# Kernel optimization log

Measured on AMD Instinct MI355X. Metric: run time of the kernel, lower is better.

Reference implementation:

```python
import jax, jax.numpy as jnp
import numpy as np

NUM_ITEMS = 50000
NUM_USERS = 16384   # static number of user segments (total_user universe)
H0 = 512            # encoder_hidden_size[0]
LAT = 256           # bottleneck (encoder_hidden_size[-1] / decoder_hidden_size[0])
N = 262144          # observed interactions
NT = 262144         # target interactions


def setup_inputs() -> dict:
    key = jax.random.key(0)
    ks = jax.random.split(key, 14)

    def glorot(k, shape):
        fan_in, fan_out = shape[1], shape[0]
        lim = np.sqrt(6.0 / (fan_in + fan_out)).astype(np.float32)
        return jax.random.uniform(k, shape, jnp.float32, -lim, lim)

    return {
        "user": jax.random.randint(ks[0], (N,), 0, NUM_USERS, jnp.int32),
        "item": jax.random.randint(ks[1], (N,), 0, NUM_ITEMS, jnp.int32),
        "rating": jax.random.normal(ks[2], (N,), jnp.float32),
        "target_user": jax.random.randint(ks[3], (NT,), 0, NUM_USERS, jnp.int32),
        "target_item": jax.random.randint(ks[4], (NT,), 0, NUM_ITEMS, jnp.int32),
        "target_rating": jax.random.normal(ks[5], (NT,), jnp.float32),
        # encoder_linear: Linear(num_items, H0)
        "W_enc": glorot(ks[6], (H0, NUM_ITEMS)),
        "b_enc": jnp.zeros((H0,), jnp.float32),
        # Encoder: Linear(H0, LAT) + Tanh
        "W1": glorot(ks[7], (LAT, H0)),
        "b1": jnp.zeros((LAT,), jnp.float32),
        # Decoder: Linear(LAT, H0) + Tanh
        "W2": glorot(ks[8], (H0, LAT)),
        "b2": jnp.zeros((H0,), jnp.float32),
        # decoder_linear: Linear(H0, num_items)
        "W_dec": glorot(ks[9], (NUM_ITEMS, H0)),
        "b_dec": jnp.zeros((NUM_ITEMS,), jnp.float32),
    }


def reference(user, item, rating, target_user, target_item, target_rating,
              W_enc, b_enc, W1, b1, W2, b2, W_dec, b_dec):
    # --- encoder: gather item weight rows, scale by rating, segment-sum per user ---
    # rows: [N, H0] gather from W_enc.T ([NUM_ITEMS, H0])
    rows = W_enc.T[item] * rating[:, None]
    # per-user aggregation over the full user universe (equivalent to the
    # torch unique/sort/index_add path: users with no interactions get 0 -> tanh(bias))
    agg = jax.ops.segment_sum(rows, user, num_segments=NUM_USERS)  # [U, H0]
    x = jnp.tanh(agg + b_enc)
    # --- small dense tanh MLP encoder/decoder ---
    encoded = jnp.tanh(x @ W1.T + b1)          # [U, LAT]
    decoded = jnp.tanh(encoded @ W2.T + b2)    # [U, H0] (dropout = identity, eval mode)
    # --- decoder: gather user codes & item decoder rows, rowwise dot ---
    g = decoded[target_user]                   # [NT, H0]
    w = W_dec[target_item]                     # [NT, H0]
    pred = jnp.sum(g * w, axis=-1) + b_dec[target_item]  # [NT]
    loss = jnp.mean((pred - target_rating) ** 2)
    return pred, loss
```

## Files before the change

### kernel.cpp

```cpp
#include <hip/hip_runtime.h>
#include <hip/hip_bf16.h>
#include <math.h>

#define NUM_ITEMS 50000
#define NUM_USERS 16384
#define H0 512
#define LAT 256
#define FP8_SCALE 64.0f
#define FP8_INV (1.0f / 64.0f)

typedef __attribute__((ext_vector_type(8))) short short8;
typedef __attribute__((ext_vector_type(4))) float floatx4;
typedef __attribute__((ext_vector_type(2))) float vf2;

__device__ __forceinline__ unsigned short f2bf(float f) {
    union { float f; unsigned i; } u; u.f = f;
    unsigned r = u.i + 0x7fff + ((u.i >> 16) & 1);
    return (unsigned short)(r >> 16);
}
__device__ __forceinline__ float bfhi(unsigned v) {
    union { unsigned i; float f; } u; u.i = v & 0xffff0000u; return u.f;
}
__device__ __forceinline__ float bflo(unsigned v) {
    union { unsigned i; float f; } u; u.i = v << 16; return u.f;
}
__device__ __forceinline__ uint4 pack8(const float* v) {
    uint4 p;
    p.x = (unsigned)f2bf(v[0]) | ((unsigned)f2bf(v[1]) << 16);
    p.y = (unsigned)f2bf(v[2]) | ((unsigned)f2bf(v[3]) << 16);
    p.z = (unsigned)f2bf(v[4]) | ((unsigned)f2bf(v[5]) << 16);
    p.w = (unsigned)f2bf(v[6]) | ((unsigned)f2bf(v[7]) << 16);
    return p;
}
__device__ __forceinline__ unsigned pkfp8_4(float a, float b, float c, float d) {
    int v = __builtin_amdgcn_cvt_pk_fp8_f32(a, b, 0, false);
    v = __builtin_amdgcn_cvt_pk_fp8_f32(c, d, v, true);
    return (unsigned)v;
}
__device__ __forceinline__ void fp8x4_to_f32(unsigned v, float* o) {
    vf2 lo = __builtin_amdgcn_cvt_pk_f32_fp8((int)v, false);
    vf2 hi = __builtin_amdgcn_cvt_pk_f32_fp8((int)v, true);
    o[0] = lo.x; o[1] = lo.y; o[2] = hi.x; o[3] = hi.y;
}

__global__ __launch_bounds__(256) void count_kernel(const int* __restrict__ user, int* __restrict__ cntU,
                                                    const int* __restrict__ t_user, int* __restrict__ cntTU,
                                                    int n, int nt) {
    int i = (blockIdx.x * blockDim.x + threadIdx.x) * 4;
    if (i + 3 < n) {
        int4 u = *(const int4*)(user + i);
        atomicAdd(&cntU[u.x], 1); atomicAdd(&cntU[u.y], 1);
        atomicAdd(&cntU[u.z], 1); atomicAdd(&cntU[u.w], 1);
    } else {
        for (int k = i; k < n; ++k) atomicAdd(&cntU[user[k]], 1);
    }
    if (i + 3 < nt) {
        int4 t = *(const int4*)(t_user + i);
        atomicAdd(&cntTU[t.x], 1); atomicAdd(&cntTU[t.y], 1);
        atomicAdd(&cntTU[t.z], 1); atomicAdd(&cntTU[t.w], 1);
    } else {
        for (int k = i; k < nt; ++k) atomicAdd(&cntTU[t_user[k]], 1);
    }
}

__device__ void scan_block(const int* __restrict__ cnt, int* __restrict__ offs,
                           int* __restrict__ cursor) {
    __shared__ int wsum_s[16];
    int t = threadIdx.x;
    int lane = t & 63, wid = t >> 6;
    int base = t * 16;
    int4 a = *(const int4*)(cnt + base);
    int4 b = *(const int4*)(cnt + base + 4);
    int4 c = *(const int4*)(cnt + base + 8);
    int4 d = *(const int4*)(cnt + base + 12);
    int s = a.x + a.y + a.z + a.w + b.x + b.y + b.z + b.w
          + c.x + c.y + c.z + c.w + d.x + d.y + d.z + d.w;
    int sc = s;
#pragma unroll
    for (int off = 1; off < 64; off <<= 1) {
        int v = __shfl_up(sc, off, 64);
        if (lane >= off) sc += v;
    }
    if (lane == 63) wsum_s[wid] = sc;
    __syncthreads();
    if (t < 16) {
        int w = wsum_s[t];
        int wsc = w;
#pragma unroll
        for (int off = 1; off < 16; off <<= 1) {
            int v = __shfl_up(wsc, off, 64);
            if (t >= off) wsc += v;
        }
        wsum_s[t] = wsc - w;
    }
    __syncthreads();
    int run = wsum_s[wid] + (sc - s);
    int4 o;
    o.x = run; run += a.x; o.y = run; run += a.y; o.z = run; run += a.z; o.w = run; run += a.w;
    *(int4*)(offs + base) = o; *(int4*)(cursor + base) = o;
    o.x = run; run += b.x; o.y = run; run += b.y; o.z = run; run += b.z; o.w = run; run += b.w;
    *(int4*)(offs + base + 4) = o; *(int4*)(cursor + base + 4) = o;
    o.x = run; run += c.x; o.y = run; run += c.y; o.z = run; run += c.z; o.w = run; run += c.w;
    *(int4*)(offs + base + 8) = o; *(int4*)(cursor + base + 8) = o;
    o.x = run; run += d.x; o.y = run; run += d.y; o.z = run; run += d.z; o.w = run; run += d.w;
    *(int4*)(offs + base + 12) = o; *(int4*)(cursor + base + 12) = o;
}

__global__ void scan_kernel(const int* __restrict__ cntU, int* __restrict__ offsU, int* __restrict__ curU,
                            const int* __restrict__ cntTU, int* __restrict__ offsTU, int* __restrict__ curTU) {
    if (blockIdx.x == 0) scan_block(cntU, offsU, curU);
    else scan_block(cntTU, offsTU, curTU);
}

__global__ __launch_bounds__(256) void scatter_kernel(
        const int* __restrict__ user, const int* __restrict__ item,
        const float* __restrict__ rating, int* __restrict__ curU, int2* __restrict__ s_pack,
        const int* __restrict__ t_user, const int* __restrict__ t_item,
        const float* __restrict__ t_rating, int* __restrict__ curTU, int4* __restrict__ st_pack,
        int n, int nt) {
    int i = blockIdx.x * 256 + threadIdx.x;
    if (i < n) {
        int u = user[i];
        int pos = atomicAdd(&curU[u], 1);
        s_pack[pos] = make_int2(item[i], __float_as_int(rating[i]));
    }
    if (i < nt) {
        int tu = t_user[i];
        int pos = atomicAdd(&curTU[tu], 1);
        st_pack[pos] = make_int4(t_item[i], __float_as_int(t_rating[i]), i, 0);
    }
}

__global__ __launch_bounds__(256) void transpose_kernel(const float* __restrict__ W_enc,
                                                        unsigned char* __restrict__ wtb8) {
    __shared__ float tileh[64 * 64];
    const int TBX = (NUM_ITEMS + 63) / 64;
    int b = blockIdx.x;
    int x0 = (b % TBX) * 64;
    int y0 = (b / TBX) * 64;
    int tid = threadIdx.x;
    int g = tid >> 4;
    int m = tid & 15;
    int it4 = x0 + m * 4;
#pragma unroll
    for (int p = 0; p < 4; ++p) {
        int hloc = p * 16 + g;
        if (it4 < NUM_ITEMS) {
            float4 v = *(const float4*)(W_enc + (size_t)(y0 + hloc) * NUM_ITEMS + it4);
            int cb = (m * 4 + ((hloc >> 2) << 2)) & 63;
            *(float4*)(tileh + hloc * 64 + cb) = v;
        }
    }
    __syncthreads();
    int i = tid >> 2;
    int l = tid & 3;
    int it = x0 + i;
    if (it < NUM_ITEMS) {
        float f[16];
#pragma unroll
        for (int k = 0; k < 16; ++k) {
            int h = l * 16 + k;
            f[k] = tileh[h * 64 + ((i + ((h >> 2) << 2)) & 63)];
        }
        uint4 o;
        o.x = pkfp8_4(f[0] * FP8_SCALE, f[1] * FP8_SCALE, f[2] * FP8_SCALE, f[3] * FP8_SCALE);
        o.y = pkfp8_4(f[4] * FP8_SCALE, f[5] * FP8_SCALE, f[6] * FP8_SCALE, f[7] * FP8_SCALE);
        o.z = pkfp8_4(f[8] * FP8_SCALE, f[9] * FP8_SCALE, f[10] * FP8_SCALE, f[11] * FP8_SCALE);
        o.w = pkfp8_4(f[12] * FP8_SCALE, f[13] * FP8_SCALE, f[14] * FP8_SCALE, f[15] * FP8_SCALE);
        *(uint4*)(wtb8 + (size_t)it * H0 + y0 + l * 16) = o;
    }
}

__global__ __launch_bounds__(256) void cast_kernel(const float* __restrict__ W_dec,
                                                   unsigned char* __restrict__ wdb8,
                                                   const float* __restrict__ W1, unsigned short* __restrict__ w1b,
                                                   const float* __restrict__ W2, unsigned short* __restrict__ w2b,
                                                   int DB) {
    int bid = blockIdx.x;
    int tid = threadIdx.x;
    if (bid < DB) {
        size_t idx = (size_t)bid * 4096 + tid * 16;
        float4 v0 = *(const float4*)(W_dec + idx);
        float4 v1 = *(const float4*)(W_dec + idx + 4);
        float4 v2 = *(const float4*)(W_dec + idx + 8);
        float4 v3 = *(const float4*)(W_dec + idx + 12);
        uint4 o;
        o.x = pkfp8_4(v0.x * FP8_SCALE, v0.y * FP8_SCALE, v0.z * FP8_SCALE, v0.w * FP8_SCALE);
        o.y = pkfp8_4(v1.x * FP8_SCALE, v1.y * FP8_SCALE, v1.z * FP8_SCALE, v1.w * FP8_SCALE);
        o.z = pkfp8_4(v2.x * FP8_SCALE, v2.y * FP8_SCALE, v2.z * FP8_SCALE, v2.w * FP8_SCALE);
        o.w = pkfp8_4(v3.x * FP8_SCALE, v3.y * FP8_SCALE, v3.z * FP8_SCALE, v3.w * FP8_SCALE);
        *(uint4*)(wdb8 + idx) = o;
    } else {
        int b2i = bid - DB;
        const float* src = (b2i < 64) ? W1 : W2;
        unsigned short* dst = (b2i < 64) ? w1b : w2b;
        int idx = (b2i & 63) * 2048 + tid * 8;
        float v[8];
        *(float4*)&v[0] = *(const float4*)(src + idx);
        *(float4*)&v[4] = *(const float4*)(src + idx + 4);
        *(uint4*)(dst + idx) = pack8(v);
    }
}

__global__ __launch_bounds__(256) void agg_kernel(const unsigned char* __restrict__ wtb8,
                                                  const int* __restrict__ offs,
                                                  const int* __restrict__ ends,
                                                  const int2* __restrict__ s_pack,
                                                  const float* __restrict__ b_enc,
                                                  unsigned short* __restrict__ xb) {
    __shared__ float red[3 * 512];
    int u = blockIdx.x;
    int tid = threadIdx.x;
    int g = tid >> 6, lane = tid & 63;
    float acc[8] = {};
    int j0 = offs[u], j1 = ends[u];
    int j = j0 + g;
    int2 c0 = (j < j1) ? s_pack[j] : make_int2(0, 0);
    int2 c1 = (j + 4 < j1) ? s_pack[j + 4] : make_int2(0, 0);
    while (j < j1) {
        bool has1 = (j + 4) < j1;
        uint2 v0 = ((const uint2*)(wtb8 + (size_t)c0.x * H0))[lane];
        uint2 v1 = has1 ? ((const uint2*)(wtb8 + (size_t)c1.x * H0))[lane] : make_uint2(0, 0);
        int jn = j + 8;
        int2 n0 = (jn < j1) ? s_pack[jn] : make_int2(0, 0);
        int2 n1 = (jn + 4 < j1) ? s_pack[jn + 4] : make_int2(0, 0);
        float r0 = __int_as_float(c0.y);
        float wf[8];
        fp8x4_to_f32(v0.x, wf);
        fp8x4_to_f32(v0.y, wf + 4);
#pragma unroll
        for (int e = 0; e < 8; ++e) acc[e] += wf[e] * r0;
        if (has1) {
            float r1 = __int_as_float(c1.y);
            fp8x4_to_f32(v1.x, wf);
            fp8x4_to_f32(v1.y, wf + 4);
#pragma unroll
            for (int e = 0; e < 8; ++e) acc[e] += wf[e] * r1;
        }
        c0 = n0; c1 = n1; j = jn;
    }
    if (g) {
        float4* rp = (float4*)red + (size_t)(g - 1) * 128 + lane * 2;
        rp[0] = make_float4(acc[0], acc[1], acc[2], acc[3]);
        rp[1] = make_float4(acc[4], acc[5], acc[6], acc[7]);
    }
    __syncthreads();
    if (g == 0) {
#pragma unroll
        for (int h = 0; h < 3; ++h) {
            const float* rp = red + h * 512 + lane * 8;
#pragma unroll
            for (int e = 0; e < 8; ++e) acc[e] += rp[e];
        }
        float4 b0 = ((const float4*)b_enc)[lane * 2];
        float4 b1 = ((const float4*)b_enc)[lane * 2 + 1];
        float o[8];
        o[0] = tanhf(acc[0] * FP8_INV + b0.x); o[1] = tanhf(acc[1] * FP8_INV + b0.y);
        o[2] = tanhf(acc[2] * FP8_INV + b0.z); o[3] = tanhf(acc[3] * FP8_INV + b0.w);
        o[4] = tanhf(acc[4] * FP8_INV + b1.x); o[5] = tanhf(acc[5] * FP8_INV + b1.y);
        o[6] = tanhf(acc[6] * FP8_INV + b1.z); o[7] = tanhf(acc[7] * FP8_INV + b1.w);
        ((uint4*)(xb + (size_t)u * H0))[lane] = pack8(o);
    }
}

template<int BN>
__global__ __launch_bounds__(256) void gemm_mfma(const unsigned short* __restrict__ A,
                                                 const unsigned short* __restrict__ B,
                                                 const float* __restrict__ bias,
                                                 unsigned short* __restrict__ C,
                                                 int Nn, int K) {
    constexpr int WN = BN / 32;
    constexpr int NCH = 8 + BN / 16;
    constexpr int PER = NCH / 4;
    __shared__ unsigned short Ash[128 * 32];
    __shared__ unsigned short Bsh[BN * 32];
    int tid = threadIdx.x;
    int wid = tid >> 6, lane = tid & 63;
    int wave_m = wid & 1, wave_n = wid >> 1;
    int quad = lane >> 4, l16 = lane & 15;
    int m0 = blockIdx.x * 128, n0 = blockIdx.y * BN;
    floatx4 acc[4][WN] = {};
    int srow = lane >> 2;
    int scol = (lane & 3) * 8;
    for (int k0 = 0; k0 < K; k0 += 32) {
#pragma unroll
        for (int i = 0; i < PER; ++i) {
            int c = wid * PER + i;
            if (c < 8) {
                const unsigned short* ga = A + (size_t)(m0 + c * 16 + srow) * K + k0 + scol;
                __builtin_amdgcn_global_load_lds(
                    (const __attribute__((address_space(1))) void*)ga,
                    (__attribute__((address_space(3))) void*)((__attribute__((address_space(3))) char*)Ash + c * 1024),
                    16, 0, 0);
            } else {
                const unsigned short* gb = B + (size_t)(n0 + (c - 8) * 16 + srow) * K + k0 + scol;
                __builtin_amdgcn_global_load_lds(
                    (const __attribute__((address_space(1))) void*)gb,
                    (__attribute__((address_space(3))) void*)((__attribute__((address_space(3))) char*)Bsh + (c - 8) * 1024),
                    16, 0, 0);
            }
        }
        __syncthreads();
        short8 af[4], bfr[WN];
#pragma unroll
        for (int i = 0; i < 4; ++i) {
            int ml = wave_m * 64 + i * 16 + l16;
            af[i] = ((const short8*)Ash)[ml * 4 + quad];
        }
#pragma unroll
        for (int j = 0; j < WN; ++j) {
            int nl = wave_n * (BN / 2) + j * 16 + l16;
            bfr[j] = ((const short8*)Bsh)[nl * 4 + quad];
        }
#pragma unroll
        for (int i = 0; i < 4; ++i)
#pragma unroll
            for (int j = 0; j < WN; ++j)
                acc[i][j] = __builtin_amdgcn_mfma_f32_16x16x32_bf16(af[i], bfr[j], acc[i][j], 0, 0, 0);
        __syncthreads();
    }
#pragma unroll
    for (int j = 0; j < WN; ++j) {
        int col = n0 + wave_n * (BN / 2) + j * 16 + l16;
        float bv = bias[col];
#pragma unroll
        for (int i = 0; i < 4; ++i) {
            int rowb = m0 + wave_m * 64 + i * 16 + quad * 4;
#pragma unroll
            for (int r = 0; r < 4; ++r)
                C[(size_t)(rowb + r) * Nn + col] = f2bf(tanhf(acc[i][j][r] + bv));
        }
    }
}

__global__ __launch_bounds__(256) void predict_kernel(const unsigned short* __restrict__ dec_b,
                                                      const unsigned char* __restrict__ wdb8,
                                                      const float* __restrict__ b_dec,
                                                      const int* __restrict__ offs,
                                                      const int* __restrict__ ends,
                                                      const int4* __restrict__ st,
                                                      float* __restrict__ pred,
                                                      float* __restrict__ partials) {
    __shared__ float wsum[4];
    int u = blockIdx.x;
    int wid = threadIdx.x >> 6, lane = threadIdx.x & 63;
    int j0 = offs[u], j1 = ends[u];
    float sq = 0.f;
    if (j0 < j1) {
        uint4 gv = ((const uint4*)(dec_b + (size_t)u * H0))[lane];
        float g[8];
        g[0] = bflo(gv.x); g[1] = bfhi(gv.x);
        g[2] = bflo(gv.y); g[3] = bfhi(gv.y);
        g[4] = bflo(gv.z); g[5] = bfhi(gv.z);
        g[6] = bflo(gv.w); g[7] = bfhi(gv.w);
        int j = j0 + wid;
        int4 tv = (j < j1) ? st[j] : make_int4(0, 0, 0, 0);
        uint2 wv = make_uint2(0, 0);
        if (j < j1) wv = ((const uint2*)(wdb8 + (size_t)tv.x * H0))[lane];
        while (j < j1) {
            int jn = j + 4;
            int4 tvn = make_int4(0, 0, 0, 0);
            uint2 wvn = make_uint2(0, 0);
            if (jn < j1) {
                tvn = st[jn];
                wvn = ((const uint2*)(wdb8 + (size_t)tvn.x * H0))[lane];
            }
            float wf[8];
            fp8x4_to_f32(wv.x, wf);
            fp8x4_to_f32(wv.y, wf + 4);
            float s = g[0] * wf[0] + g[1] * wf[1] + g[2] * wf[2] + g[3] * wf[3]
                    + g[4] * wf[4] + g[5] * wf[5] + g[6] * wf[6] + g[7] * wf[7];
#pragma unroll
            for (int off = 32; off; off >>= 1) s += __shfl_xor(s, off, 64);
            if (lane == 0) {
                float p = s * FP8_INV + b_dec[tv.x];
                pred[tv.z] = p;
                float d = p - __int_as_float(tv.y);
                sq += d * d;
            }
            j = jn; tv = tvn; wv = wvn;
        }
    }
    if (lane == 0) wsum[wid] = sq;
    __syncthreads();
    if (threadIdx.x == 0)
        partials[u] = wsum[0] + wsum[1] + wsum[2] + wsum[3];
}

__global__ void loss_reduce(const float* __restrict__ partials, float* __restrict__ out_loss,
                            int nPart, float invNT) {
    __shared__ float s[256];
    int t = threadIdx.x;
    float a = 0.f;
    const float4* p4 = (const float4*)partials;
    int n4 = nPart >> 2;
    for (int i = t; i < n4; i += 256) {
        float4 v = p4[i];
        a += v.x + v.y + v.z + v.w;
    }
    for (int i = (n4 << 2) + t; i < nPart; i += 256) a += partials[i];
    s[t] = a;
    __syncthreads();
    for (int off = 128; off; off >>= 1) {
        if (t < off) s[t] += s[t + off];
        __syncthreads();
    }
    if (t == 0) out_loss[0] = s[0] * invNT;
}

extern "C" void kernel_launch(void* const* d_in, const int* in_sizes, int n_in,
                              void* d_out, int out_size, void* d_ws, size_t ws_size,
                              hipStream_t stream) {
    const int* user = (const int*)d_in[0];
    const int* item = (const int*)d_in[1];
    const float* rating = (const float*)d_in[2];
    const int* t_user = (const int*)d_in[3];
    const int* t_item = (const int*)d_in[4];
    const float* t_rating = (const float*)d_in[5];
    const float* W_enc = (const float*)d_in[6];
    const float* b_enc = (const float*)d_in[7];
    const float* W1 = (const float*)d_in[8];
    const float* b1 = (const float*)d_in[9];
    const float* W2 = (const float*)d_in[10];
    const float* b2 = (const float*)d_in[11];
    const float* W_dec = (const float*)d_in[12];
    const float* b_dec = (const float*)d_in[13];
    const int N = in_sizes[0];
    const int NT = in_sizes[3];

    char* ws = (char*)d_ws;
    size_t off = 0;
    auto alloc = [&](size_t bytes) {
        void* p = ws + off;
        off = (off + bytes + 255) & ~(size_t)255;
        return p;
    };
    unsigned char* wtb8 = (unsigned char*)alloc((size_t)NUM_ITEMS * H0);
    unsigned char* wdb8 = (unsigned char*)alloc((size_t)NUM_ITEMS * H0);
    unsigned short* xb = (unsigned short*)alloc((size_t)NUM_USERS * H0 * 2);
    unsigned short* enc_b = (unsigned short*)alloc((size_t)NUM_USERS * LAT * 2);
    unsigned short* dec_b = (unsigned short*)alloc((size_t)NUM_USERS * H0 * 2);
    unsigned short* w1b = (unsigned short*)alloc((size_t)LAT * H0 * 2);
    unsigned short* w2b = (unsigned short*)alloc((size_t)H0 * LAT * 2);
    int* cntU = (int*)alloc((size_t)NUM_USERS * 2 * 4);
    int* cntTU = cntU + NUM_USERS;
    int* offsU = (int*)alloc((size_t)NUM_USERS * 4);
    int* curU = (int*)alloc((size_t)NUM_USERS * 4);
    int* offsTU = (int*)alloc((size_t)NUM_USERS * 4);
    int* curTU = (int*)alloc((size_t)NUM_USERS * 4);
    int2* s_pack = (int2*)alloc((size_t)N * 8);
    int4* st_pack = (int4*)alloc((size_t)NT * 16);
    float* partials = (float*)alloc((size_t)NUM_USERS * 4);

    float* pred = (float*)d_out;
    float* loss = pred + NT;

    const int maxNNT = N > NT ? N : NT;
    const int SB = (maxNNT + 255) / 256;
    const int TBX = (NUM_ITEMS + 63) / 64;
    const int TB = TBX * (H0 / 64);
    const int DB = (NUM_ITEMS * H0) / 4096;
    const int WB = 128;

    hipMemsetAsync(cntU, 0, (size_t)NUM_USERS * 2 * 4, stream);
    count_kernel<<<(maxNNT + 1023) / 1024, 256, 0, stream>>>(user, cntU, t_user, cntTU, N, NT);
    scan_kernel<<<2, 1024, 0, stream>>>(cntU, offsU, curU, cntTU, offsTU, curTU);
    scatter_kernel<<<SB, 256, 0, stream>>>(user, item, rating, curU, s_pack,
                                           t_user, t_item, t_rating, curTU, st_pack, N, NT);
    transpose_kernel<<<TB, 256, 0, stream>>>(W_enc, wtb8);
    cast_kernel<<<DB + WB, 256, 0, stream>>>(W_dec, wdb8, W1, w1b, W2, w2b, DB);
    agg_kernel<<<NUM_USERS, 256, 0, stream>>>(wtb8, offsU, curU, s_pack, b_enc, xb);
    gemm_mfma<64><<<dim3(NUM_USERS / 128, LAT / 64), 256, 0, stream>>>(xb, w1b, b1, enc_b, LAT, H0);
    gemm_mfma<64><<<dim3(NUM_USERS / 128, H0 / 64), 256, 0, stream>>>(enc_b, w2b, b2, dec_b, H0, LAT);
    predict_kernel<<<NUM_USERS, 256, 0, stream>>>(dec_b, wdb8, b_dec, offsTU, curTU, st_pack, pred, partials);
    loss_reduce<<<1, 256, 0, stream>>>(partials, loss, NUM_USERS, 1.0f / NT);
}
```

Baseline: 427.8 us.

## Process four targets per wavefront in predict and widen transpose tiles

The predict kernel now splits each wavefront into four 16-lane groups, each handling one target row with 32-byte loads, so a wave covers four interactions per iteration and only needs a 4-step shuffle reduction. The software prefetch of the next row is dropped. The transpose kernel uses 64x128 tiles with no LDS swizzle and writes 32 bytes per thread. The unswizzled column reads in the transpose may cause LDS bank conflicts, and the per-user loop can leave groups idle when a user has few targets.

```diff
diff --git a/kernel.cpp b/kernel.cpp
--- a/kernel.cpp
+++ b/kernel.cpp
@@ -41,6 +41,12 @@
     vf2 lo = __builtin_amdgcn_cvt_pk_f32_fp8((int)v, false);
     vf2 hi = __builtin_amdgcn_cvt_pk_f32_fp8((int)v, true);
     o[0] = lo.x; o[1] = lo.y; o[2] = hi.x; o[3] = hi.y;
+}
+__device__ __forceinline__ void unpbf8(uint4 q, float* o) {
+    o[0] = bflo(q.x); o[1] = bfhi(q.x);
+    o[2] = bflo(q.y); o[3] = bfhi(q.y);
+    o[4] = bflo(q.z); o[5] = bfhi(q.z);
+    o[6] = bflo(q.w); o[7] = bfhi(q.w);
 }
 
 __global__ __launch_bounds__(256) void count_kernel(const int* __restrict__ user, int* __restrict__ cntU,
@@ -133,41 +139,44 @@
 
 __global__ __launch_bounds__(256) void transpose_kernel(const float* __restrict__ W_enc,
                                                         unsigned char* __restrict__ wtb8) {
-    __shared__ float tileh[64 * 64];
-    const int TBX = (NUM_ITEMS + 63) / 64;
+    __shared__ float tileh[64 * 128];
+    const int TBX = (NUM_ITEMS + 127) / 128;
     int b = blockIdx.x;
-    int x0 = (b % TBX) * 64;
+    int x0 = (b % TBX) * 128;
     int y0 = (b / TBX) * 64;
     int tid = threadIdx.x;
-    int g = tid >> 4;
-    int m = tid & 15;
+    int g = tid >> 5;
+    int m = tid & 31;
     int it4 = x0 + m * 4;
 #pragma unroll
-    for (int p = 0; p < 4; ++p) {
-        int hloc = p * 16 + g;
+    for (int p = 0; p < 8; ++p) {
+        int hloc = p * 8 + g;
         if (it4 < NUM_ITEMS) {
             float4 v = *(const float4*)(W_enc + (size_t)(y0 + hloc) * NUM_ITEMS + it4);
-            int cb = (m * 4 + ((hloc >> 2) << 2)) & 63;
-            *(float4*)(tileh + hloc * 64 + cb) = v;
-        }
-    }
-    __syncthreads();
-    int i = tid >> 2;
-    int l = tid & 3;
+            *(float4*)(tileh + hloc * 128 + m * 4) = v;
+        }
+    }
+    __syncthreads();
+    int i = tid >> 1;
+    int l = tid & 1;
     int it = x0 + i;
     if (it < NUM_ITEMS) {
-        float f[16];
-#pragma unroll
-        for (int k = 0; k < 16; ++k) {
-            int h = l * 16 + k;
-            f[k] = tileh[h * 64 + ((i + ((h >> 2) << 2)) & 63)];
-        }
-        uint4 o;
-        o.x = pkfp8_4(f[0] * FP8_SCALE, f[1] * FP8_SCALE, f[2] * FP8_SCALE, f[3] * FP8_SCALE);
-        o.y = pkfp8_4(f[4] * FP8_SCALE, f[5] * FP8_SCALE, f[6] * FP8_SCALE, f[7] * FP8_SCALE);
-        o.z = pkfp8_4(f[8] * FP8_SCALE, f[9] * FP8_SCALE, f[10] * FP8_SCALE, f[11] * FP8_SCALE);
-        o.w = pkfp8_4(f[12] * FP8_SCALE, f[13] * FP8_SCALE, f[14] * FP8_SCALE, f[15] * FP8_SCALE);
-        *(uint4*)(wtb8 + (size_t)it * H0 + y0 + l * 16) = o;
+        float f[32];
+#pragma unroll
+        for (int k = 0; k < 32; ++k)
+            f[k] = tileh[(l * 32 + k) * 128 + i];
+        uint4 o0, o1;
+        o0.x = pkfp8_4(f[0] * FP8_SCALE, f[1] * FP8_SCALE, f[2] * FP8_SCALE, f[3] * FP8_SCALE);
+        o0.y = pkfp8_4(f[4] * FP8_SCALE, f[5] * FP8_SCALE, f[6] * FP8_SCALE, f[7] * FP8_SCALE);
+        o0.z = pkfp8_4(f[8] * FP8_SCALE, f[9] * FP8_SCALE, f[10] * FP8_SCALE, f[11] * FP8_SCALE);
+        o0.w = pkfp8_4(f[12] * FP8_SCALE, f[13] * FP8_SCALE, f[14] * FP8_SCALE, f[15] * FP8_SCALE);
+        o1.x = pkfp8_4(f[16] * FP8_SCALE, f[17] * FP8_SCALE, f[18] * FP8_SCALE, f[19] * FP8_SCALE);
+        o1.y = pkfp8_4(f[20] * FP8_SCALE, f[21] * FP8_SCALE, f[22] * FP8_SCALE, f[23] * FP8_SCALE);
+        o1.z = pkfp8_4(f[24] * FP8_SCALE, f[25] * FP8_SCALE, f[26] * FP8_SCALE, f[27] * FP8_SCALE);
+        o1.w = pkfp8_4(f[28] * FP8_SCALE, f[29] * FP8_SCALE, f[30] * FP8_SCALE, f[31] * FP8_SCALE);
+        unsigned char* dst = wtb8 + (size_t)it * H0 + y0 + l * 32;
+        *(uint4*)dst = o0;
+        *(uint4*)(dst + 16) = o1;
     }
 }
 
@@ -344,43 +353,46 @@
     __shared__ float wsum[4];
     int u = blockIdx.x;
     int wid = threadIdx.x >> 6, lane = threadIdx.x & 63;
+    int grp = lane >> 4, sl = lane & 15;
     int j0 = offs[u], j1 = ends[u];
     float sq = 0.f;
     if (j0 < j1) {
-        uint4 gv = ((const uint4*)(dec_b + (size_t)u * H0))[lane];
-        float g[8];
-        g[0] = bflo(gv.x); g[1] = bfhi(gv.x);
-        g[2] = bflo(gv.y); g[3] = bfhi(gv.y);
-        g[4] = bflo(gv.z); g[5] = bfhi(gv.z);
-        g[6] = bflo(gv.w); g[7] = bfhi(gv.w);
-        int j = j0 + wid;
-        int4 tv = (j < j1) ? st[j] : make_int4(0, 0, 0, 0);
-        uint2 wv = make_uint2(0, 0);
-        if (j < j1) wv = ((const uint2*)(wdb8 + (size_t)tv.x * H0))[lane];
-        while (j < j1) {
-            int jn = j + 4;
-            int4 tvn = make_int4(0, 0, 0, 0);
-            uint2 wvn = make_uint2(0, 0);
-            if (jn < j1) {
-                tvn = st[jn];
-                wvn = ((const uint2*)(wdb8 + (size_t)tvn.x * H0))[lane];
+        const uint4* gp = (const uint4*)(dec_b + (size_t)u * H0) + sl * 4;
+        float g[32];
+        unpbf8(gp[0], g);
+        unpbf8(gp[1], g + 8);
+        unpbf8(gp[2], g + 16);
+        unpbf8(gp[3], g + 24);
+        for (int base = j0 + wid * 4; base < j1; base += 16) {
+            int idx = base + grp;
+            bool act = idx < j1;
+            int4 tv = st[min(idx, j1 - 1)];
+            const unsigned char* wr = wdb8 + (size_t)tv.x * H0 + sl * 32;
+            uint4 wa = *(const uint4*)wr;
+            uint4 wb = *(const uint4*)(wr + 16);
+            unsigned wu[8] = {wa.x, wa.y, wa.z, wa.w, wb.x, wb.y, wb.z, wb.w};
+            float s = 0.f;
+#pragma unroll
+            for (int q = 0; q < 8; ++q) {
+                float wf[4];
+                fp8x4_to_f32(wu[q], wf);
+                s += g[q * 4 + 0] * wf[0] + g[q * 4 + 1] * wf[1]
+                   + g[q * 4 + 2] * wf[2] + g[q * 4 + 3] * wf[3];
             }
-            float wf[8];
-            fp8x4_to_f32(wv.x, wf);
-            fp8x4_to_f32(wv.y, wf + 4);
-            float s = g[0] * wf[0] + g[1] * wf[1] + g[2] * wf[2] + g[3] * wf[3]
-                    + g[4] * wf[4] + g[5] * wf[5] + g[6] * wf[6] + g[7] * wf[7];
-#pragma unroll
-            for (int off = 32; off; off >>= 1) s += __shfl_xor(s, off, 64);
-            if (lane == 0) {
+            s += __shfl_xor(s, 1, 64);
+            s += __shfl_xor(s, 2, 64);
+            s += __shfl_xor(s, 4, 64);
+            s += __shfl_xor(s, 8, 64);
+            if (act && sl == 0) {
                 float p = s * FP8_INV + b_dec[tv.x];
                 pred[tv.z] = p;
                 float d = p - __int_as_float(tv.y);
                 sq += d * d;
             }
-            j = jn; tv = tvn; wv = wvn;
-        }
-    }
+        }
+    }
+    sq += __shfl_xor(sq, 16, 64);
+    sq += __shfl_xor(sq, 32, 64);
     if (lane == 0) wsum[wid] = sq;
     __syncthreads();
     if (threadIdx.x == 0)
@@ -457,7 +469,7 @@
 
     const int maxNNT = N > NT ? N : NT;
     const int SB = (maxNNT + 255) / 256;
-    const int TBX = (NUM_ITEMS + 63) / 64;
+    const int TBX = (NUM_ITEMS + 127) / 128;
     const int TB = TBX * (H0 / 64);
     const int DB = (NUM_ITEMS * H0) / 4096;
     const int WB = 128;
```

Measured after the change: 416.2 us. 2.7% less time.
